# Optimization experiments

Measured on AMD Instinct MI355X. Metric: run time of the kernel, lower is better.

Reference implementation:

```python
import jax, jax.numpy as jnp
import numpy as np

B, N_DET, N_T, NY, NX = 4, 128, 2048, 256, 256


def setup_inputs() -> dict:
    key = jax.random.key(0)
    k1, k2, k3 = jax.random.split(key, 3)
    sino = jax.random.normal(k1, (B, 1, N_DET, N_T), dtype=jnp.float32)
    # LUT channel 0: floor temporal index (stored as float, cast to int in forward)
    k_floor = jax.random.randint(k2, (NY, NX, N_DET), 0, N_T).astype(jnp.float32)
    # LUT channel 1: linear interpolation weight alpha in [0,1)
    alpha = jax.random.uniform(k3, (NY, NX, N_DET), dtype=jnp.float32)
    lut = jnp.stack([k_floor, alpha], axis=-1)  # [NY, NX, N_DET, 2]
    return {"sino": sino, "lut": lut}


def reference(sino, lut):
    # sino: [B, 1, n_det, n_t]; lut: [ny, nx, n_det, 2]
    b, c, n_det, n_t = sino.shape
    k_floor = lut[..., 0].astype(jnp.int32)          # [ny, nx, n_det]
    alpha = lut[..., 1]                               # [ny, nx, n_det]
    valid = (k_floor >= 0) & (k_floor < n_t - 1)
    k0 = jnp.clip(k_floor, 0, n_t - 2)
    k1 = k0 + 1
    S = sino[:, 0]                                    # [B, n_det, n_t]
    det = jnp.arange(n_det)                           # broadcasts against [ny,nx,n_det]
    s0 = S[:, det, k0]                                # [B, ny, nx, n_det]
    s1 = S[:, det, k1]                                # [B, ny, nx, n_det]
    sk = (1.0 - alpha) * s0 + alpha * s1
    sk = jnp.where(valid, sk, jnp.zeros_like(sk))
    # Hann apodization window over detectors
    apod = (0.5 - 0.5 * jnp.cos(2.0 * jnp.pi * jnp.arange(n_det, dtype=jnp.float32)
                                / max(n_det - 1, 1))).astype(sino.dtype)
    out = jnp.einsum('bijd,d->bij', sk, apod)
    norm = jnp.maximum(apod.sum(), 1e-06)
    out = out / norm
    return out[:, None]                               # [B, 1, ny, nx]
```

## Files before the change

### kernel.cpp

```cpp
#include <hip/hip_runtime.h>
#include <hip/hip_fp16.h>


#define NB      4
#define NDET    128
#define NT      2048
#define NPIX    65536
#define DPH     4
#define NPHASE  2
#define DBLOCK  (DPH * NPHASE)
#define PTILE   2048
#define THREADS 512
#define PXPT    (PTILE / THREADS)

__global__ __launch_bounds__(THREADS, 4)
void bp_kernel(const float* __restrict__ sino,
               const float* __restrict__ lut,
               float* __restrict__ out) {
    __shared__ __half2 lds[DPH][2][NT];

    const int tid   = threadIdx.x;
    const int octet = blockIdx.x & 15;
    const int tile  = blockIdx.x >> 4;
    const int d0    = octet * DBLOCK;
    const int px0   = tile * PTILE;

    float apod[DBLOCK];
#pragma unroll
    for (int j = 0; j < DBLOCK; ++j) {
        float x = (float)(d0 + j) * (6.28318530717958647692f / 127.0f);
        apod[j] = 0.5f - 0.5f * __cosf(x);
    }

    float4 L[PXPT][4];
#pragma unroll
    for (int i = 0; i < PXPT; ++i) {
        const float4* lp = (const float4*)
            (lut + ((size_t)(px0 + tid + i * THREADS) * NDET + d0) * 2);
#pragma unroll
        for (int q = 0; q < 4; ++q) L[i][q] = lp[q];
    }

    float acc[PXPT][NB];
#pragma unroll
    for (int i = 0; i < PXPT; ++i)
#pragma unroll
        for (int b = 0; b < NB; ++b) acc[i][b] = 0.0f;

    for (int phase = 0; phase < NPHASE; ++phase) {
        const int dg0 = d0 + phase * DPH;
        if (phase) __syncthreads();

        for (int f = tid; f < DPH * NT; f += THREADS) {
            int dl = f >> 11;
            int t  = f & (NT - 1);
            const float* src = sino + ((size_t)(dg0 + dl) * NT + t);
            float v0 = src[0];
            float v1 = src[(size_t)1 * NDET * NT];
            float v2 = src[(size_t)2 * NDET * NT];
            float v3 = src[(size_t)3 * NDET * NT];
            lds[dl][0][t] = __floats2half2_rn(v0, v1);
            lds[dl][1][t] = __floats2half2_rn(v2, v3);
        }
        __syncthreads();

#pragma unroll
        for (int i = 0; i < PXPT; ++i) {
#pragma unroll
            for (int q = 0; q < 2; ++q) {
                float4 Lq = L[i][phase * 2 + q];
#pragma unroll
                for (int h = 0; h < 2; ++h) {
                    float kf = h ? Lq.z : Lq.x;
                    float af = h ? Lq.w : Lq.y;
                    int   dl = q * 2 + h;
                    int   j  = phase * DPH + dl;

                    int k = (int)kf;
                    unsigned uk = (unsigned)k;
                    bool valid = uk < (unsigned)(NT - 1);
                    float w  = valid ? apod[j] : 0.0f;
                    int  k0  = valid ? k : 0;
                    __half2 A  = lds[dl][0][k0];
                    __half2 Bv = lds[dl][0][k0 + 1];
                    __half2 C  = lds[dl][1][k0];
                    __half2 Dv = lds[dl][1][k0 + 1];
                    __half2 a2 = __float2half2_rn(af);
                    __half2 s01 = __hfma2(a2, __hsub2(Bv, A), A);
                    __half2 s23 = __hfma2(a2, __hsub2(Dv, C), C);
                    float2 f01 = __half22float2(s01);
                    float2 f23 = __half22float2(s23);
                    acc[i][0] = fmaf(w, f01.x, acc[i][0]);
                    acc[i][1] = fmaf(w, f01.y, acc[i][1]);
                    acc[i][2] = fmaf(w, f23.x, acc[i][2]);
                    acc[i][3] = fmaf(w, f23.y, acc[i][3]);
                }
            }
        }
    }

    const float inv_norm = 1.0f / 63.5f;
#pragma unroll
    for (int i = 0; i < PXPT; ++i) {
        const int px = px0 + tid + i * THREADS;
#pragma unroll
        for (int b = 0; b < NB; ++b) {
            atomicAdd(&out[(size_t)b * NPIX + px], acc[i][b] * inv_norm);
        }
    }
}

extern "C" void kernel_launch(void* const* d_in, const int* in_sizes, int n_in,
                              void* d_out, int out_size, void* d_ws, size_t ws_size,
                              hipStream_t stream) {
    const float* sino = (const float*)d_in[0];
    const float* lut  = (const float*)d_in[1];
    float* out = (float*)d_out;

    hipMemsetAsync(d_out, 0, (size_t)out_size * sizeof(float), stream);

    bp_kernel<<<dim3(512), dim3(THREADS), 0, stream>>>(sino, lut, out);
}
```

Measured before the change: 139.8 us.

## Stage all 8 detectors for a batch pair per phase, halve pixel tile

Each phase now loads all eight detectors of the block into LDS for one pair of batches, instead of four detectors for all four batches. The staging loop reads contiguous float4 rows of the sinogram, replacing four strided scalar loads per element. The pixel tile is halved and the grid doubled to 1024 blocks, giving more parallelism. In exchange each LUT entry's index and weight are decoded twice, the per-lookup gathers are narrower, and the sinogram is loaded twice as often overall.

```diff
diff --git a/kernel.cpp b/kernel.cpp
--- a/kernel.cpp
+++ b/kernel.cpp
@@ -6,10 +6,9 @@
 #define NDET    128
 #define NT      2048
 #define NPIX    65536
-#define DPH     4
+#define DBLOCK  8
 #define NPHASE  2
-#define DBLOCK  (DPH * NPHASE)
-#define PTILE   2048
+#define PTILE   1024
 #define THREADS 512
 #define PXPT    (PTILE / THREADS)
 
@@ -17,7 +16,7 @@
 void bp_kernel(const float* __restrict__ sino,
                const float* __restrict__ lut,
                float* __restrict__ out) {
-    __shared__ __half2 lds[DPH][2][NT];
+    __shared__ __half2 lds[DBLOCK][NT];
 
     const int tid   = threadIdx.x;
     const int octet = blockIdx.x & 15;
@@ -47,53 +46,47 @@
 #pragma unroll
         for (int b = 0; b < NB; ++b) acc[i][b] = 0.0f;
 
-    for (int phase = 0; phase < NPHASE; ++phase) {
-        const int dg0 = d0 + phase * DPH;
-        if (phase) __syncthreads();
+    for (int ph = 0; ph < NPHASE; ++ph) {
+        const int b0 = ph * 2;
+        if (ph) __syncthreads();
 
-        for (int f = tid; f < DPH * NT; f += THREADS) {
-            int dl = f >> 11;
-            int t  = f & (NT - 1);
-            const float* src = sino + ((size_t)(dg0 + dl) * NT + t);
-            float v0 = src[0];
-            float v1 = src[(size_t)1 * NDET * NT];
-            float v2 = src[(size_t)2 * NDET * NT];
-            float v3 = src[(size_t)3 * NDET * NT];
-            lds[dl][0][t] = __floats2half2_rn(v0, v1);
-            lds[dl][1][t] = __floats2half2_rn(v2, v3);
+        for (int f = tid; f < DBLOCK * (NT / 4); f += THREADS) {
+            int dl = f >> 9;
+            int t4 = f & 511;
+            const float4* s4 = (const float4*)sino;
+            float4 ve = s4[((size_t)(b0 + 0) * NDET + (d0 + dl)) * (NT / 4) + t4];
+            float4 vo = s4[((size_t)(b0 + 1) * NDET + (d0 + dl)) * (NT / 4) + t4];
+            __half2* dst = &lds[dl][t4 * 4];
+            dst[0] = __floats2half2_rn(ve.x, vo.x);
+            dst[1] = __floats2half2_rn(ve.y, vo.y);
+            dst[2] = __floats2half2_rn(ve.z, vo.z);
+            dst[3] = __floats2half2_rn(ve.w, vo.w);
         }
         __syncthreads();
 
 #pragma unroll
         for (int i = 0; i < PXPT; ++i) {
 #pragma unroll
-            for (int q = 0; q < 2; ++q) {
-                float4 Lq = L[i][phase * 2 + q];
+            for (int q = 0; q < 4; ++q) {
+                float4 Lq = L[i][q];
 #pragma unroll
                 for (int h = 0; h < 2; ++h) {
                     float kf = h ? Lq.z : Lq.x;
                     float af = h ? Lq.w : Lq.y;
                     int   dl = q * 2 + h;
-                    int   j  = phase * DPH + dl;
 
                     int k = (int)kf;
                     unsigned uk = (unsigned)k;
                     bool valid = uk < (unsigned)(NT - 1);
-                    float w  = valid ? apod[j] : 0.0f;
+                    float w  = valid ? apod[dl] : 0.0f;
                     int  k0  = valid ? k : 0;
-                    __half2 A  = lds[dl][0][k0];
-                    __half2 Bv = lds[dl][0][k0 + 1];
-                    __half2 C  = lds[dl][1][k0];
-                    __half2 Dv = lds[dl][1][k0 + 1];
+                    __half2 s0 = lds[dl][k0];
+                    __half2 s1 = lds[dl][k0 + 1];
                     __half2 a2 = __float2half2_rn(af);
-                    __half2 s01 = __hfma2(a2, __hsub2(Bv, A), A);
-                    __half2 s23 = __hfma2(a2, __hsub2(Dv, C), C);
-                    float2 f01 = __half22float2(s01);
-                    float2 f23 = __half22float2(s23);
-                    acc[i][0] = fmaf(w, f01.x, acc[i][0]);
-                    acc[i][1] = fmaf(w, f01.y, acc[i][1]);
-                    acc[i][2] = fmaf(w, f23.x, acc[i][2]);
-                    acc[i][3] = fmaf(w, f23.y, acc[i][3]);
+                    __half2 sk = __hfma2(a2, __hsub2(s1, s0), s0);
+                    float2  fv = __half22float2(sk);
+                    acc[i][b0 + 0] = fmaf(w, fv.x, acc[i][b0 + 0]);
+                    acc[i][b0 + 1] = fmaf(w, fv.y, acc[i][b0 + 1]);
                 }
             }
         }
@@ -119,5 +112,5 @@
 
     hipMemsetAsync(d_out, 0, (size_t)out_size * sizeof(float), stream);
 
-    bp_kernel<<<dim3(512), dim3(THREADS), 0, stream>>>(sino, lut, out);
+    bp_kernel<<<dim3(1024), dim3(THREADS), 0, stream>>>(sino, lut, out);
 }
```

New measurement: 129.7 us. -7.2%, faster.
